# Optimization experiments

Measured on AMD Instinct MI355X. Metric: run time of the kernel, lower is better.

The kernel has to match this reference:

```python
import jax, jax.numpy as jnp
import numpy as np

NUM_LAYERS = 4
HIDDEN = 32
INPUT = 2
B = 16384
T = 64


def setup_inputs() -> dict:
    key = jax.random.key(0)
    ks = jax.random.split(key, 8)
    s = 1.0 / np.sqrt(HIDDEN)  # PyTorch LSTM default init scale
    return {
        "x": jax.random.normal(ks[0], (B, 3, T), dtype=jnp.float32),
        "W_ih0": jax.random.uniform(ks[1], (4 * HIDDEN, INPUT), minval=-s, maxval=s, dtype=jnp.float32),
        "W_ih": jax.random.uniform(ks[2], (NUM_LAYERS - 1, 4 * HIDDEN, HIDDEN), minval=-s, maxval=s, dtype=jnp.float32),
        "W_hh": jax.random.uniform(ks[3], (NUM_LAYERS, 4 * HIDDEN, HIDDEN), minval=-s, maxval=s, dtype=jnp.float32),
        "b_ih": jax.random.uniform(ks[4], (NUM_LAYERS, 4 * HIDDEN), minval=-s, maxval=s, dtype=jnp.float32),
        "b_hh": jax.random.uniform(ks[5], (NUM_LAYERS, 4 * HIDDEN), minval=-s, maxval=s, dtype=jnp.float32),
        "W_lin": jax.random.uniform(ks[6], (1, HIDDEN), minval=-s, maxval=s, dtype=jnp.float32),
        "b_lin": jax.random.uniform(ks[7], (1,), minval=-s, maxval=s, dtype=jnp.float32),
    }


def _lstm_cell(inp, h, c, Wih, Whh, b):
    # inp: [B, in_dim]; h, c: [B, H]; Wih: [4H, in_dim]; Whh: [4H, H]; b: [4H]
    gates = inp @ Wih.T + h @ Whh.T + b  # [B, 4H]
    i, f, g, o = jnp.split(gates, 4, axis=-1)  # PyTorch gate order: i, f, g, o
    i = jax.nn.sigmoid(i)
    f = jax.nn.sigmoid(f)
    g = jnp.tanh(g)
    o = jax.nn.sigmoid(o)
    c_new = f * c + i * g
    h_new = o * jnp.tanh(c_new)
    return h_new, c_new


def reference(x, W_ih0, W_ih, W_hh, b_ih, b_hh, W_lin, b_lin):
    # x: [B, 3, T]; channel 2 (id) is discarded, as in the original forward.
    feats = x[:, :2, :]                         # [B, 2, T]
    xs = jnp.transpose(feats, (2, 0, 1))        # [T, B, 2]
    bsz = x.shape[0]
    h0 = jnp.zeros((NUM_LAYERS, bsz, HIDDEN), dtype=x.dtype)
    c0 = jnp.zeros((NUM_LAYERS, bsz, HIDDEN), dtype=x.dtype)
    bias = b_ih + b_hh  # [L, 4H]

    def step(carry, xt):
        h, c = carry  # each [L, B, H]
        inp = xt
        hs, cs = [], []
        for l in range(NUM_LAYERS):
            Wih = W_ih0 if l == 0 else W_ih[l - 1]
            h_new, c_new = _lstm_cell(inp, h[l], c[l], Wih, W_hh[l], bias[l])
            hs.append(h_new)
            cs.append(c_new)
            inp = h_new
        return (jnp.stack(hs), jnp.stack(cs)), None

    (h, c), _ = jax.lax.scan(step, (h0, c0), xs)
    # last timestep's top-layer output -> linear -> sigmoid -> squeeze to [B]
    out = jax.nn.sigmoid(h[-1] @ W_lin.T + b_lin)  # [B, 1]
    return out.squeeze(-1)
```

## Files before the change

### kernel.cpp

```cpp
#include <hip/hip_runtime.h>

typedef float  f32x4  __attribute__((ext_vector_type(4)));
typedef short  bf16x8 __attribute__((ext_vector_type(8)));

#define LOG2E    1.4426950408889634f
#define TWOLOG2E 2.8853900817779268f

__device__ __forceinline__ unsigned short f2b(float f) {
    unsigned int u = __builtin_bit_cast(unsigned int, f);
    u += 0x7fffu + ((u >> 16) & 1u);
    return (unsigned short)(u >> 16);
}
__device__ __forceinline__ float b2f(unsigned short s) {
    unsigned int u = ((unsigned int)s) << 16;
    return __builtin_bit_cast(float, u);
}
__device__ __forceinline__ float sig2(float xh) {
    return __builtin_amdgcn_rcpf(1.0f + __builtin_amdgcn_exp2f(-xh));
}
__device__ __forceinline__ float th2(float xh) {
    return 2.0f * __builtin_amdgcn_rcpf(1.0f + __builtin_amdgcn_exp2f(-xh)) - 1.0f;
}
__device__ __forceinline__ float thc(float c) {
    return 2.0f * __builtin_amdgcn_rcpf(1.0f + __builtin_amdgcn_exp2f(c * -TWOLOG2E)) - 1.0f;
}

__global__ void pack_weights(const float* __restrict__ Wih0, const float* __restrict__ Wih,
                             const float* __restrict__ Whh,  const float* __restrict__ bih,
                             const float* __restrict__ bhh,  void* __restrict__ wsv) {
    short* wsb = (short*)wsv;
    float* bsf = (float*)((char*)wsv + 65536);
    int idx = blockIdx.x * 256 + threadIdx.x;
    if (idx < 32768) {
        int k = idx & 63, G = (idx >> 6) & 127, l = idx >> 13;
        float scale = ((G >> 5) == 2) ? TWOLOG2E : LOG2E;
        float v = 0.0f;
        if (l == 0) {
            if (k < 2)        v = Wih0[G * 2 + k];
            else if (k >= 32) v = Whh[G * 32 + (k - 32)];
        } else {
            v = (k < 32) ? Wih[(l - 1) * 4096 + G * 32 + k]
                         : Whh[l * 4096 + G * 32 + (k - 32)];
        }
        wsb[idx] = (short)f2b(v * scale);
    } else if (idx < 33280) {
        int r = idx - 32768;
        int G = r & 127, l = r >> 7;
        float scale = ((G >> 5) == 2) ? TWOLOG2E : LOG2E;
        bsf[r] = (bih[l * 128 + G] + bhh[l * 128 + G]) * scale;
    }
}

__global__ __launch_bounds__(256, 2)
void lstm_mfma(const float* __restrict__ xg, const void* __restrict__ wsv,
               const float* __restrict__ Wlin, const float* __restrict__ blin,
               float* __restrict__ out) {
    __shared__ short        hb[4 * 2 * 1280] __attribute__((aligned(16)));
    __shared__ unsigned int xb[64 * 32];

    const short* wsb = (const short*)wsv;
    const float* bsf = (const float*)((const char*)wsv + 65536);

    const int tid  = threadIdx.x;
    const int wv   = __builtin_amdgcn_readfirstlane(tid >> 6);
    const int lane = tid & 63;
    const int m    = lane & 15;
    const int q    = lane >> 4;
    const int row0 = blockIdx.x * 32;

    for (int i = tid; i < 5120; i += 256) ((unsigned int*)hb)[i] = 0u;

    for (int i = tid; i < 2048; i += 256) {
        int r = i >> 6, t = i & 63;
        float x0 = xg[(size_t)(row0 + r) * 192 + t];
        float x1 = xg[(size_t)(row0 + r) * 192 + 64 + t];
        xb[t * 32 + r] = (unsigned int)f2b(x0) | ((unsigned int)f2b(x1) << 16);
    }

    bf16x8 bfr[8][2];
#pragma unroll
    for (int g = 0; g < 8; ++g)
#pragma unroll
        for (int c = 0; c < 2; ++c)
            bfr[g][c] = *(const bf16x8*)(wsb + ((wv * 128 + g * 16 + m) * 64 + c * 32 + q * 8));

    float bias_v[8];
#pragma unroll
    for (int g = 0; g < 8; ++g) bias_v[g] = bsf[wv * 128 + g * 16 + m];

    float cst[2][2][4];
#pragma unroll
    for (int tt = 0; tt < 2; ++tt)
#pragma unroll
        for (int u = 0; u < 2; ++u)
#pragma unroll
            for (int r = 0; r < 4; ++r) cst[tt][u][r] = 0.0f;

    __syncthreads();

    for (int s = 0; s < 67; ++s) {
        const int t = s - wv;
        if (t >= 0 && t < 64) {
            const int rp = (s - 1) & 1;
            const int wp = s & 1;
            short*       hw    = hb + (wv * 2 + wp) * 1280;
            const short* hrin  = hb + (((wv > 0 ? wv - 1 : 0) * 2) + rp) * 1280;
            const short* hrrec = hb + (wv * 2 + rp) * 1280;
#pragma unroll
            for (int tt = 0; tt < 2; ++tt) {
                bf16x8 a0;
                if (wv == 0) {
                    unsigned int xd = xb[t * 32 + tt * 16 + m];
                    bf16x8 z = (bf16x8)0;
                    a0 = z;
                    if (q == 0) { a0[0] = (short)(xd & 0xffffu); a0[1] = (short)(xd >> 16); }
                } else {
                    a0 = *(const bf16x8*)(hrin + (tt * 16 + m) * 40 + q * 8);
                }
                bf16x8 a1 = *(const bf16x8*)(hrrec + (tt * 16 + m) * 40 + q * 8);

                f32x4 acc[8];
#pragma unroll
                for (int g = 0; g < 8; ++g) {
                    f32x4 zz = {0.f, 0.f, 0.f, 0.f};
                    acc[g] = __builtin_amdgcn_mfma_f32_16x16x32_bf16(a0, bfr[g][0], zz, 0, 0, 0);
                    acc[g] = __builtin_amdgcn_mfma_f32_16x16x32_bf16(a1, bfr[g][1], acc[g], 0, 0, 0);
                }
#pragma unroll
                for (int r = 0; r < 4; ++r) {
                    float iA = sig2(acc[0][r] + bias_v[0]);
                    float fA = sig2(acc[2][r] + bias_v[2]);
                    float gA = th2 (acc[4][r] + bias_v[4]);
                    float oA = sig2(acc[6][r] + bias_v[6]);
                    float cA = fA * cst[tt][0][r] + iA * gA;
                    cst[tt][0][r] = cA;
                    float hA = oA * thc(cA);

                    float iB = sig2(acc[1][r] + bias_v[1]);
                    float fB = sig2(acc[3][r] + bias_v[3]);
                    float gB = th2 (acc[5][r] + bias_v[5]);
                    float oB = sig2(acc[7][r] + bias_v[7]);
                    float cB = fB * cst[tt][1][r] + iB * gB;
                    cst[tt][1][r] = cB;
                    float hB = oB * thc(cB);

                    int rowi = tt * 16 + q * 4 + r;
                    hw[rowi * 40 + m]      = (short)f2b(hA);
                    hw[rowi * 40 + m + 16] = (short)f2b(hB);
                }
            }
        }
        __syncthreads();
    }

    if (tid < 32) {
        const short* h3 = hb + (3 * 2 + 0) * 1280;
        float s = blin[0];
#pragma unroll
        for (int k = 0; k < 32; ++k)
            s += Wlin[k] * b2f((unsigned short)h3[tid * 40 + k]);
        out[row0 + tid] = sig2(s * LOG2E);
    }
}

extern "C" void kernel_launch(void* const* d_in, const int* in_sizes, int n_in,
                              void* d_out, int out_size, void* d_ws, size_t ws_size,
                              hipStream_t stream) {
    const float* x    = (const float*)d_in[0];
    const float* Wih0 = (const float*)d_in[1];
    const float* Wih  = (const float*)d_in[2];
    const float* Whh  = (const float*)d_in[3];
    const float* bih  = (const float*)d_in[4];
    const float* bhh  = (const float*)d_in[5];
    const float* Wlin = (const float*)d_in[6];
    const float* blin = (const float*)d_in[7];
    float* out = (float*)d_out;

    pack_weights<<<130, 256, 0, stream>>>(Wih0, Wih, Whh, bih, bhh, d_ws);
    lstm_mfma<<<512, 256, 0, stream>>>(x, d_ws, Wlin, blin, out);
}
```

Before: 244.1 us.

## Halve rows per block, fuse weight packing, interleave hidden columns for packed stores

Each block now handles 16 batch rows instead of 32, launching 1024 blocks with launch bounds raised to 4 blocks per SM. The intent is more parallelism and occupancy to hide the serial recurrence latency. The separate pack_weights kernel is removed: each wave converts and scales its fp32 weights to bf16 fragments in place, saving a launch at the cost of redundant per-block conversion. Gate rows are interleaved so a lane owns two adjacent hidden units and can write h as one packed 32-bit store.

```diff
diff --git a/kernel.cpp b/kernel.cpp
--- a/kernel.cpp
+++ b/kernel.cpp
@@ -15,6 +15,9 @@
     unsigned int u = ((unsigned int)s) << 16;
     return __builtin_bit_cast(float, u);
 }
+__device__ __forceinline__ unsigned int pk2(float lo, float hi) {
+    return (unsigned int)f2b(lo) | ((unsigned int)f2b(hi) << 16);
+}
 __device__ __forceinline__ float sig2(float xh) {
     return __builtin_amdgcn_rcpf(1.0f + __builtin_amdgcn_exp2f(-xh));
 }
@@ -25,136 +28,129 @@
     return 2.0f * __builtin_amdgcn_rcpf(1.0f + __builtin_amdgcn_exp2f(c * -TWOLOG2E)) - 1.0f;
 }
 
-__global__ void pack_weights(const float* __restrict__ Wih0, const float* __restrict__ Wih,
-                             const float* __restrict__ Whh,  const float* __restrict__ bih,
-                             const float* __restrict__ bhh,  void* __restrict__ wsv) {
-    short* wsb = (short*)wsv;
-    float* bsf = (float*)((char*)wsv + 65536);
-    int idx = blockIdx.x * 256 + threadIdx.x;
-    if (idx < 32768) {
-        int k = idx & 63, G = (idx >> 6) & 127, l = idx >> 13;
-        float scale = ((G >> 5) == 2) ? TWOLOG2E : LOG2E;
-        float v = 0.0f;
-        if (l == 0) {
-            if (k < 2)        v = Wih0[G * 2 + k];
-            else if (k >= 32) v = Whh[G * 32 + (k - 32)];
-        } else {
-            v = (k < 32) ? Wih[(l - 1) * 4096 + G * 32 + k]
-                         : Whh[l * 4096 + G * 32 + (k - 32)];
-        }
-        wsb[idx] = (short)f2b(v * scale);
-    } else if (idx < 33280) {
-        int r = idx - 32768;
-        int G = r & 127, l = r >> 7;
-        float scale = ((G >> 5) == 2) ? TWOLOG2E : LOG2E;
-        bsf[r] = (bih[l * 128 + G] + bhh[l * 128 + G]) * scale;
-    }
-}
-
-__global__ __launch_bounds__(256, 2)
-void lstm_mfma(const float* __restrict__ xg, const void* __restrict__ wsv,
-               const float* __restrict__ Wlin, const float* __restrict__ blin,
+__global__ __launch_bounds__(256, 4)
+void lstm_mfma(const float* __restrict__ xg,  const float* __restrict__ Wih0,
+               const float* __restrict__ Wih, const float* __restrict__ Whh,
+               const float* __restrict__ bih, const float* __restrict__ bhh,
+               const float* __restrict__ Wlin,const float* __restrict__ blin,
                float* __restrict__ out) {
-    __shared__ short        hb[4 * 2 * 1280] __attribute__((aligned(16)));
-    __shared__ unsigned int xb[64 * 32];
-
-    const short* wsb = (const short*)wsv;
-    const float* bsf = (const float*)((const char*)wsv + 65536);
+    __shared__ short        hb[4 * 2 * 640] __attribute__((aligned(16)));
+    __shared__ unsigned int xb[64 * 16];
 
     const int tid  = threadIdx.x;
     const int wv   = __builtin_amdgcn_readfirstlane(tid >> 6);
     const int lane = tid & 63;
     const int m    = lane & 15;
     const int q    = lane >> 4;
-    const int row0 = blockIdx.x * 32;
+    const int row0 = blockIdx.x * 16;
 
-    for (int i = tid; i < 5120; i += 256) ((unsigned int*)hb)[i] = 0u;
+    for (int i = tid; i < 2560; i += 256) ((unsigned int*)hb)[i] = 0u;
 
-    for (int i = tid; i < 2048; i += 256) {
+    for (int i = tid; i < 1024; i += 256) {
         int r = i >> 6, t = i & 63;
         float x0 = xg[(size_t)(row0 + r) * 192 + t];
         float x1 = xg[(size_t)(row0 + r) * 192 + 64 + t];
-        xb[t * 32 + r] = (unsigned int)f2b(x0) | ((unsigned int)f2b(x1) << 16);
+        xb[t * 16 + r] = pk2(x0, x1);
     }
 
     bf16x8 bfr[8][2];
+    float  bv[8];
 #pragma unroll
-    for (int g = 0; g < 8; ++g)
+    for (int g = 0; g < 8; ++g) {
+        const int   T    = g >> 1;
+        const int   rowG = T * 32 + 2 * m + (g & 1);
+        const float sc   = (T == 2) ? TWOLOG2E : LOG2E;
+        bv[g] = (bih[wv * 128 + rowG] + bhh[wv * 128 + rowG]) * sc;
 #pragma unroll
-        for (int c = 0; c < 2; ++c)
-            bfr[g][c] = *(const bf16x8*)(wsb + ((wv * 128 + g * 16 + m) * 64 + c * 32 + q * 8));
+        for (int c = 0; c < 2; ++c) {
+            const int k0 = c * 32 + q * 8;
+            float w[8];
+            if (wv == 0) {
+                if (c == 0) {
+#pragma unroll
+                    for (int jj = 0; jj < 8; ++jj) w[jj] = 0.0f;
+                    if (q == 0) { w[0] = Wih0[rowG * 2]; w[1] = Wih0[rowG * 2 + 1]; }
+                } else {
+                    const float* src = Whh + rowG * 32 + (k0 - 32);
+#pragma unroll
+                    for (int jj = 0; jj < 8; ++jj) w[jj] = src[jj];
+                }
+            } else {
+                const float* src = (c == 0) ? (Wih + (wv - 1) * 4096 + rowG * 32 + k0)
+                                            : (Whh + wv * 4096 + rowG * 32 + (k0 - 32));
+#pragma unroll
+                for (int jj = 0; jj < 8; ++jj) w[jj] = src[jj];
+            }
+            bf16x8 fr;
+#pragma unroll
+            for (int jj = 0; jj < 8; ++jj) fr[jj] = (short)f2b(w[jj] * sc);
+            bfr[g][c] = fr;
+        }
+    }
 
-    float bias_v[8];
+    float cst[2][4];
 #pragma unroll
-    for (int g = 0; g < 8; ++g) bias_v[g] = bsf[wv * 128 + g * 16 + m];
-
-    float cst[2][2][4];
+    for (int hf = 0; hf < 2; ++hf)
 #pragma unroll
-    for (int tt = 0; tt < 2; ++tt)
-#pragma unroll
-        for (int u = 0; u < 2; ++u)
-#pragma unroll
-            for (int r = 0; r < 4; ++r) cst[tt][u][r] = 0.0f;
+        for (int r = 0; r < 4; ++r) cst[hf][r] = 0.0f;
 
     __syncthreads();
 
     for (int s = 0; s < 67; ++s) {
         const int t = s - wv;
         if (t >= 0 && t < 64) {
-            const int rp = (s - 1) & 1;
+            const int rp = (s + 1) & 1;
             const int wp = s & 1;
-            short*       hw    = hb + (wv * 2 + wp) * 1280;
-            const short* hrin  = hb + (((wv > 0 ? wv - 1 : 0) * 2) + rp) * 1280;
-            const short* hrrec = hb + (wv * 2 + rp) * 1280;
+            const short* hrin  = hb + ((wv > 0 ? wv - 1 : 0) * 2 + rp) * 640;
+            const short* hrrec = hb + (wv * 2 + rp) * 640;
+            short*       hw    = hb + (wv * 2 + wp) * 640;
+
+            bf16x8 a0, a1;
+            if (wv == 0) {
+                unsigned int xd = xb[t * 16 + m];
+                unsigned int lo = (q == 0) ? xd : 0u;
+                union { unsigned int u[4]; bf16x8 v; } au;
+                au.u[0] = lo; au.u[1] = 0u; au.u[2] = 0u; au.u[3] = 0u;
+                a0 = au.v;
+            } else {
+                a0 = *(const bf16x8*)(hrin + m * 40 + q * 8);
+            }
+            a1 = *(const bf16x8*)(hrrec + m * 40 + q * 8);
+
+            float h0[4];
 #pragma unroll
-            for (int tt = 0; tt < 2; ++tt) {
-                bf16x8 a0;
-                if (wv == 0) {
-                    unsigned int xd = xb[t * 32 + tt * 16 + m];
-                    bf16x8 z = (bf16x8)0;
-                    a0 = z;
-                    if (q == 0) { a0[0] = (short)(xd & 0xffffu); a0[1] = (short)(xd >> 16); }
-                } else {
-                    a0 = *(const bf16x8*)(hrin + (tt * 16 + m) * 40 + q * 8);
-                }
-                bf16x8 a1 = *(const bf16x8*)(hrrec + (tt * 16 + m) * 40 + q * 8);
-
-                f32x4 acc[8];
-#pragma unroll
-                for (int g = 0; g < 8; ++g) {
-                    f32x4 zz = {0.f, 0.f, 0.f, 0.f};
-                    acc[g] = __builtin_amdgcn_mfma_f32_16x16x32_bf16(a0, bfr[g][0], zz, 0, 0, 0);
-                    acc[g] = __builtin_amdgcn_mfma_f32_16x16x32_bf16(a1, bfr[g][1], acc[g], 0, 0, 0);
-                }
+            for (int hf = 0; hf < 2; ++hf) {
+                f32x4 zz = {0.f, 0.f, 0.f, 0.f};
+                f32x4 ai = __builtin_amdgcn_mfma_f32_16x16x32_bf16(a0, bfr[0 + hf][0], zz, 0, 0, 0);
+                ai       = __builtin_amdgcn_mfma_f32_16x16x32_bf16(a1, bfr[0 + hf][1], ai, 0, 0, 0);
+                f32x4 af = __builtin_amdgcn_mfma_f32_16x16x32_bf16(a0, bfr[2 + hf][0], zz, 0, 0, 0);
+                af       = __builtin_amdgcn_mfma_f32_16x16x32_bf16(a1, bfr[2 + hf][1], af, 0, 0, 0);
+                f32x4 ag = __builtin_amdgcn_mfma_f32_16x16x32_bf16(a0, bfr[4 + hf][0], zz, 0, 0, 0);
+                ag       = __builtin_amdgcn_mfma_f32_16x16x32_bf16(a1, bfr[4 + hf][1], ag, 0, 0, 0);
+                f32x4 ao = __builtin_amdgcn_mfma_f32_16x16x32_bf16(a0, bfr[6 + hf][0], zz, 0, 0, 0);
+                ao       = __builtin_amdgcn_mfma_f32_16x16x32_bf16(a1, bfr[6 + hf][1], ao, 0, 0, 0);
 #pragma unroll
                 for (int r = 0; r < 4; ++r) {
-                    float iA = sig2(acc[0][r] + bias_v[0]);
-                    float fA = sig2(acc[2][r] + bias_v[2]);
-                    float gA = th2 (acc[4][r] + bias_v[4]);
-                    float oA = sig2(acc[6][r] + bias_v[6]);
-                    float cA = fA * cst[tt][0][r] + iA * gA;
-                    cst[tt][0][r] = cA;
-                    float hA = oA * thc(cA);
-
-                    float iB = sig2(acc[1][r] + bias_v[1]);
-                    float fB = sig2(acc[3][r] + bias_v[3]);
-                    float gB = th2 (acc[5][r] + bias_v[5]);
-                    float oB = sig2(acc[7][r] + bias_v[7]);
-                    float cB = fB * cst[tt][1][r] + iB * gB;
-                    cst[tt][1][r] = cB;
-                    float hB = oB * thc(cB);
-
-                    int rowi = tt * 16 + q * 4 + r;
-                    hw[rowi * 40 + m]      = (short)f2b(hA);
-                    hw[rowi * 40 + m + 16] = (short)f2b(hB);
+                    float i_ = sig2(ai[r] + bv[0 + hf]);
+                    float f_ = sig2(af[r] + bv[2 + hf]);
+                    float g_ = th2 (ag[r] + bv[4 + hf]);
+                    float o_ = sig2(ao[r] + bv[6 + hf]);
+                    float cn = f_ * cst[hf][r] + i_ * g_;
+                    cst[hf][r] = cn;
+                    float hh = o_ * thc(cn);
+                    if (hf == 0) {
+                        h0[r] = hh;
+                    } else {
+                        ((unsigned int*)hw)[(q * 4 + r) * 20 + m] = pk2(h0[r], hh);
+                    }
                 }
             }
         }
         __syncthreads();
     }
 
-    if (tid < 32) {
-        const short* h3 = hb + (3 * 2 + 0) * 1280;
+    if (tid < 16) {
+        const short* h3 = hb + (3 * 2 + 0) * 640;
         float s = blin[0];
 #pragma unroll
         for (int k = 0; k < 32; ++k)
@@ -176,6 +172,5 @@
     const float* blin = (const float*)d_in[7];
     float* out = (float*)d_out;
 
-    pack_weights<<<130, 256, 0, stream>>>(Wih0, Wih, Whh, bih, bhh, d_ws);
-    lstm_mfma<<<512, 256, 0, stream>>>(x, d_ws, Wlin, blin, out);
+    lstm_mfma<<<1024, 256, 0, stream>>>(x, Wih0, Wih, Whh, bih, bhh, Wlin, blin, out);
 }
```

New measurement: 261.7 us. 1.07x slower.
